# Performance work log

Hardware: AMD Instinct MI355X
Metric: run time of the kernel (lower is better)

## Reference

```python
import jax, jax.numpy as jnp
import numpy as np

B, N_PTS, M_ROIS = 2, 8192, 2048
C_IN, O, H, NS = 128, 256, 4, 32
RADIUS = 1.6
BN_EPS = 1e-5
SCALE = 10.0  # point cloud extent


def setup_inputs() -> dict:
    key = jax.random.key(0)
    ks = jax.random.split(key, 20)
    f32 = jnp.float32
    Cg = C_IN + 3  # grouper concats relative xyz to features

    def kaiming(k, shape, fan_in):
        return jax.random.normal(k, shape, f32) * np.sqrt(2.0 / fan_in)

    inp = {
        "xyz": jax.random.uniform(ks[0], (B, N_PTS, 3), f32) * SCALE,
        "new_xyz": jax.random.uniform(ks[1], (B, M_ROIS, 3), f32) * SCALE,
        "features": jax.random.normal(ks[2], (B, C_IN, N_PTS), f32),
        # conv1d (kernel=1, no bias) weights, torch layout (out, in)
        "pos_w": kaiming(ks[3], (O, 3), 3),
        "key_w": kaiming(ks[4], (O, Cg), Cg),
        "val_w1": kaiming(ks[5], (O, Cg), Cg),
        "bn1_g": jnp.ones((O,), f32), "bn1_b": jnp.zeros((O,), f32),
        "val_w2": kaiming(ks[6], (O, O), O),
        "bn2_g": jnp.ones((O,), f32), "bn2_b": jnp.zeros((O,), f32),
        "attn_w": kaiming(ks[7], (H, O), O),
        # sigmoid-gated coefficient linears (no bias)
        "kc_w": kaiming(ks[8], (O, O), O),
        "qc_w": kaiming(ks[9], (O, O), O),
        "qkc_w": kaiming(ks[10], (O, O), O),
        "vc_w": kaiming(ks[11], (O, O), O),
        # cls/reg weight MLPs: Linear(O,O//2)+ReLU, Linear(O//2,1)+Sigmoid
        "cls_w1": kaiming(ks[12], (O // 2, O), O), "cls_b1": jnp.zeros((O // 2,), f32),
        "cls_w2": kaiming(ks[13], (1, O // 2), O // 2), "cls_b2": jnp.zeros((1,), f32),
        "reg_w1": kaiming(ks[14], (O // 2, O), O), "reg_b1": jnp.zeros((O // 2,), f32),
        "reg_w2": kaiming(ks[15], (1, O // 2), O // 2), "reg_b2": jnp.zeros((1,), f32),
    }
    return inp


def _bn(x, g, b):
    # eval-mode BatchNorm1d with running_mean=0, running_var=1 (init state)
    return g[None, :, None] * (x * (1.0 / np.sqrt(1.0 + BN_EPS))) + b[None, :, None]


def _conv1x1(w, x):  # (O,C) x (M,C,NS) -> (M,O,NS)
    return jnp.einsum('oc,mcn->mon', w, x)


def _ball_group(pts, q):
    # ball query: first NS points within RADIUS of each query (pad with first hit)
    n_tot = pts.shape[0]
    d2 = jnp.sum((q[:, None, :] - pts[None, :, :]) ** 2, axis=-1)  # (M, Ntot)
    order = jnp.where(d2 < RADIUS ** 2, jnp.arange(n_tot, dtype=jnp.int32), n_tot)
    neg_vals, idx = jax.lax.top_k(-order, NS)  # smallest indices among in-ball pts
    valid = (-neg_vals) < n_tot
    idx = jnp.where(valid, idx, idx[:, :1])  # pad with first neighbor
    has_any = valid[:, :1]
    idx = jnp.where(has_any, idx, 0)  # empty balls -> point 0
    return idx, ~has_any[:, 0]


def reference(xyz, new_xyz, features, pos_w, key_w, val_w1, bn1_g, bn1_b,
              val_w2, bn2_g, bn2_b, attn_w, kc_w, qc_w, qkc_w, vc_w,
              cls_w1, cls_b1, cls_w2, cls_b2, reg_w1, reg_b1, reg_w2, reg_b2):
    pts = xyz.reshape(-1, 3)                                   # (Ntot, 3)
    feats = features.transpose(0, 2, 1).reshape(-1, C_IN)      # (Ntot, C)
    q = new_xyz.reshape(-1, 3)                                 # (M, 3)

    idx, empty_mask = _ball_group(pts, q)                      # (M, NS)
    gx = pts[idx] - q[:, None, :]                              # relative xyz (M,NS,3)
    gxt = gx.transpose(0, 2, 1)                                # (M,3,NS)
    gf = jnp.concatenate([gx, feats[idx]], axis=-1).transpose(0, 2, 1)  # (M,C+3,NS)

    pos = jax.nn.relu(_conv1x1(pos_w, gxt))                    # (M,O,NS)
    key = jax.nn.relu(_conv1x1(key_w, gf))                     # (M,O,NS)
    v = jax.nn.relu(_bn(_conv1x1(val_w1, gf), bn1_g, bn1_b))
    val = jax.nn.relu(_bn(_conv1x1(val_w2, v), bn2_g, bn2_b))  # (M,O,NS)
    pos_key = pos * key

    sig = jax.nn.sigmoid
    v_c = sig(pos.mean(2) @ vc_w.T)                            # (M,O)
    q_c = sig(pos.mean(2) @ qc_w.T)
    k_c = sig(key.mean(2) @ kc_w.T)
    qk_c = sig(pos_key.mean(2) @ qkc_w.T)

    val = val + pos * v_c[:, :, None]
    attn_emb = pos * q_c[:, :, None] + key * k_c[:, :, None] + pos_key * qk_c[:, :, None]
    attn = jax.nn.softmax(jnp.einsum('ho,mon->mhn', attn_w, attn_emb), axis=-1)  # (M,H,NS)

    m = val.shape[0]
    vh = val.reshape(m, H, O // H, NS)
    new_features = jnp.einsum('mhdn,mhn->mhd', vh, attn).reshape(m, O)  # (M,O)

    def gate(x, w1, b1, w2, b2):
        return sig(jax.nn.relu(x @ w1.T + b1) @ w2.T + b2)

    cls_features = new_features * gate(new_features, cls_w1, cls_b1, cls_w2, cls_b2)
    reg_features = new_features * gate(new_features, reg_w1, reg_b1, reg_w2, reg_b2)
    return new_features, cls_features, reg_features
```

## Files before the change

kernel.cpp:

```cpp
#include <hip/hip_runtime.h>

#define DI __device__ __forceinline__

typedef __attribute__((ext_vector_type(8))) short bf16x8;
typedef __attribute__((ext_vector_type(4))) short s16x4;
typedef __attribute__((ext_vector_type(4))) float f32x4;

DI short f2bs(float x){ unsigned u = __float_as_uint(x);
  return (short)((u + 0x7FFF + ((u >> 16) & 1)) >> 16); }
DI float bs2f(short s){ return __uint_as_float(((unsigned)(unsigned short)s) << 16); }
DI f32x4 MFMA(bf16x8 a, bf16x8 b, f32x4 c){
  return __builtin_amdgcn_mfma_f32_16x16x32_bf16(a, b, c, 0, 0, 0);
}

constexpr int NP   = 8192;
constexpr int NTOT = 16384;
constexpr int M    = 4096;
constexpr int C    = 128;
constexpr int O    = 256;
constexpr int NS   = 32;
constexpr int H    = 4;
constexpr int KP   = 160;
constexpr int GFS  = 168;
constexpr int VS   = 264;
constexpr int NSP  = 34;
constexpr float BNS = 0.99999500003749969f;

__global__ __launch_bounds__(256) void k_prep(
    const float* __restrict__ feat,
    const float* __restrict__ kw, const float* __restrict__ v1w,
    const float* __restrict__ v2w,
    const float* __restrict__ vcw, const float* __restrict__ qcw,
    const float* __restrict__ kcw, const float* __restrict__ qkcw,
    const float* __restrict__ cw1, const float* __restrict__ rw1,
    const float* __restrict__ xyz, const float* __restrict__ nxyz,
    short* __restrict__ fT,
    short* __restrict__ keyP, short* __restrict__ v1P,
    short* __restrict__ v2b,
    short* __restrict__ gw,
    short* __restrict__ cw1b, short* __restrict__ rw1b,
    float* __restrict__ xyz4, float* __restrict__ nxyz4)
{
  __shared__ float tile[128][65];
  int blk = blockIdx.x;
  int t = threadIdx.x;
  if(blk < 256){
    int b  = blk >> 7;
    int n0 = (blk & 127) << 6;
    int nn = t & 63, c4 = t >> 6;
    const float* src = feat + (size_t)b * C * NP;
    for(int i = 0; i < 32; i++){
      int c = c4 * 32 + i;
      tile[c][nn] = src[(size_t)c * NP + n0 + nn];
    }
    __syncthreads();
    int c2 = t & 127, nb = t >> 7;
    for(int j = 0; j < 32; j++){
      int n = nb + j * 2;
      fT[((size_t)(b * NP + n0 + n)) * C + c2] = f2bs(tile[c2][n]);
    }
    return;
  }
  int i = (blk - 256) * 256 + t;
  if(i < O * KP){
    int o = i / KP, k = i % KP;
    float a = 0.0f, b = 0.0f;
    if(k < 128){ a = kw[o*131 + 3 + k]; b = v1w[o*131 + 3 + k]; }
    else if(k < 131){ a = kw[o*131 + (k - 128)]; b = v1w[o*131 + (k - 128)]; }
    keyP[i] = f2bs(a);
    v1P[i]  = f2bs(b);
  }
  if(i < O * O){
    v2b[i] = f2bs(v2w[i]);
    gw[0*O*O + i] = f2bs(vcw[i]);
    gw[1*O*O + i] = f2bs(qcw[i]);
    gw[2*O*O + i] = f2bs(kcw[i]);
    gw[3*O*O + i] = f2bs(qkcw[i]);
  }
  if(i < (O/2) * O){
    cw1b[i] = f2bs(cw1[i]);
    rw1b[i] = f2bs(rw1[i]);
  }
  if(i < NTOT){
    xyz4[i*4+0] = xyz[i*3+0];
    xyz4[i*4+1] = xyz[i*3+1];
    xyz4[i*4+2] = xyz[i*3+2];
    xyz4[i*4+3] = 0.0f;
  }
  if(i < M){
    nxyz4[i*4+0] = nxyz[i*3+0];
    nxyz4[i*4+1] = nxyz[i*3+1];
    nxyz4[i*4+2] = nxyz[i*3+2];
    nxyz4[i*4+3] = 0.0f;
  }
}

__global__ __launch_bounds__(256) void k_ballq(const float* __restrict__ xyz4,
                                               const float* __restrict__ nxyz4,
                                               int* __restrict__ idxo,
                                               float* __restrict__ gxo){
#pragma clang fp contract(off)
  int m = blockIdx.x;
  int t = threadIdx.x;
  int w = t >> 6, lane = t & 63;
  float qx = nxyz4[m*4+0], qy = nxyz4[m*4+1], qz = nxyz4[m*4+2];
  __shared__ int sel[NS];
  __shared__ int wcnt[2][4];
  int cnt = 0;
  int par = 0;
  for(int base = 0; base < NTOT; base += 256){
    int p = base + t;
    const float4 pt = *(const float4*)(xyz4 + (size_t)p*4);
    float dx = qx - pt.x, dy = qy - pt.y, dz = qz - pt.z;
    float d2 = dx*dx + dy*dy;
    d2 = d2 + dz*dz;
    bool pred = d2 < 2.56f;
    unsigned long long bal = __ballot(pred);
    if(lane == 0) wcnt[par][w] = __popcll(bal);
    __syncthreads();
    int c0 = wcnt[par][0], c1 = wcnt[par][1], c2 = wcnt[par][2], c3 = wcnt[par][3];
    int off = cnt + ((w > 0) ? c0 : 0) + ((w > 1) ? c1 : 0) + ((w > 2) ? c2 : 0);
    if(pred){
      int pos = off + __popcll(bal & ((1ull << lane) - 1ull));
      if(pos < NS) sel[pos] = p;
    }
    cnt += c0 + c1 + c2 + c3;
    par ^= 1;
    if(cnt >= NS) break;
  }
  __syncthreads();
  if(t < NS){
    int s = 0;
    if(cnt > 0) s = (t < cnt) ? sel[t] : sel[0];
    idxo[m*NS + t] = s;
    const float4 ps = *(const float4*)(xyz4 + (size_t)s*4);
    gxo[(m*NS+t)*3+0] = ps.x - qx;
    gxo[(m*NS+t)*3+1] = ps.y - qy;
    gxo[(m*NS+t)*3+2] = ps.z - qz;
  }
}

__global__ __launch_bounds__(256, 5) void k_conv(
    const short* __restrict__ fT,
    const short* __restrict__ keyP, const short* __restrict__ v1P,
    const short* __restrict__ v2b,
    const float* __restrict__ posw,
    const float* __restrict__ g1, const float* __restrict__ b1,
    const float* __restrict__ g2, const float* __restrict__ b2,
    const int* __restrict__ idxw, const float* __restrict__ gxw,
    short* __restrict__ keyT, short* __restrict__ valT,
    short* __restrict__ mPos, short* __restrict__ mKey, short* __restrict__ mPK,
    int q0)
{
  int lq = blockIdx.x, q = q0 + lq, t = threadIdx.x;
  int w = t >> 6, l = t & 63;
  int col = l & 15, kq = l >> 4;
  int ro = w * 64;
  __shared__ __align__(16) short gf[NS * GFS];
  __shared__ __align__(16) short buf[O * NSP];
  __shared__ float gxs[NS * 4];
  __shared__ int  sel[NS];
  if(t < NS){
    sel[t] = idxw[q*NS + t];
    gxs[t*4+0] = gxw[(q*NS+t)*3+0];
    gxs[t*4+1] = gxw[(q*NS+t)*3+1];
    gxs[t*4+2] = gxw[(q*NS+t)*3+2];
    gxs[t*4+3] = 0.0f;
  }
  __syncthreads();
  for(int i = 0; i < 8; i++){
    int n = w*8 + i;
    int p = sel[n];
    *(unsigned*)&gf[n*GFS + l*2] = *(const unsigned*)(fT + (size_t)p * C + l*2);
  }
  {
    int n = t & 31, kk = (t >> 5) * 4;
    for(int j = 0; j < 4; j++){
      int k = kk + j;
      float v = (k < 3) ? gxs[n*4 + k] : 0.0f;
      gf[n*GFS + 128 + k] = f2bs(v);
    }
  }
  __syncthreads();

  f32x4 acc[4][2];
  const f32x4 vzero = {0.0f, 0.0f, 0.0f, 0.0f};

  for(int mt=0;mt<4;mt++) for(int nt=0;nt<2;nt++) acc[mt][nt] = vzero;
  for(int ks = 0; ks < 5; ks++){
    bf16x8 b0 = *(const bf16x8*)&gf[col*GFS + ks*32 + kq*8];
    bf16x8 b1v = *(const bf16x8*)&gf[(16+col)*GFS + ks*32 + kq*8];
    for(int mt = 0; mt < 4; mt++){
      bf16x8 a = *(const bf16x8*)(keyP + (size_t)(ro + mt*16 + col)*KP + ks*32 + kq*8);
      acc[mt][0] = MFMA(a, b0, acc[mt][0]);
      acc[mt][1] = MFMA(a, b1v, acc[mt][1]);
    }
  }
  for(int mt=0;mt<4;mt++) for(int nt=0;nt<2;nt++)
    for(int r=0;r<4;r++){
      int o = ro + mt*16 + kq*4 + r;
      int n = nt*16 + col;
      buf[o*NSP + n] = f2bs(fmaxf(acc[mt][nt][r], 0.0f));
    }
  for(int mt=0;mt<4;mt++){
    for(int r=0;r<4;r++){
      int o = ro + mt*16 + kq*4 + r;
      float w0 = posw[o*3+0], w1 = posw[o*3+1], w2 = posw[o*3+2];
      float sp = 0, sk = 0, spk = 0;
      for(int nt=0;nt<2;nt++){
        int n = nt*16 + col;
        float p = fmaxf(w0*gxs[n*4+0] + w1*gxs[n*4+1] + w2*gxs[n*4+2], 0.0f);
        float v = fmaxf(acc[mt][nt][r], 0.0f);
        sp += p; sk += v; spk += p*v;
      }
      for(int msk=1; msk<16; msk<<=1){
        sp += __shfl_xor(sp, msk); sk += __shfl_xor(sk, msk); spk += __shfl_xor(spk, msk);
      }
      if(col == 0){
        mPos[lq*O+o] = f2bs(sp  * 0.03125f);
        mKey[lq*O+o] = f2bs(sk  * 0.03125f);
        mPK [lq*O+o] = f2bs(spk * 0.03125f);
      }
    }
  }
  __syncthreads();
  {
    uint vv[16];
    #pragma unroll
    for(int j=0;j<16;j++) vv[j] = *(const uint*)&buf[t*NSP + j*2];
    uint4* dst = (uint4*)(keyT + ((size_t)lq*O + t)*NS);
    dst[0] = make_uint4(vv[0],vv[1],vv[2],vv[3]);
    dst[1] = make_uint4(vv[4],vv[5],vv[6],vv[7]);
    dst[2] = make_uint4(vv[8],vv[9],vv[10],vv[11]);
    dst[3] = make_uint4(vv[12],vv[13],vv[14],vv[15]);
  }

  for(int mt=0;mt<4;mt++) for(int nt=0;nt<2;nt++) acc[mt][nt] = vzero;
  for(int ks = 0; ks < 5; ks++){
    bf16x8 b0 = *(const bf16x8*)&gf[col*GFS + ks*32 + kq*8];
    bf16x8 b1v = *(const bf16x8*)&gf[(16+col)*GFS + ks*32 + kq*8];
    for(int mt = 0; mt < 4; mt++){
      bf16x8 a = *(const bf16x8*)(v1P + (size_t)(ro + mt*16 + col)*KP + ks*32 + kq*8);
      acc[mt][0] = MFMA(a, b0, acc[mt][0]);
      acc[mt][1] = MFMA(a, b1v, acc[mt][1]);
    }
  }
  __syncthreads();
  for(int mt=0;mt<4;mt++){
    int o0 = ro + mt*16 + kq*4;
    float gg[4], bb[4];
    for(int r=0;r<4;r++){ gg[r] = g1[o0+r]; bb[r] = b1[o0+r]; }
    for(int nt=0;nt<2;nt++){
      s16x4 pk;
      for(int r=0;r<4;r++)
        pk[r] = f2bs(fmaxf(gg[r]*(acc[mt][nt][r] * BNS) + bb[r], 0.0f));
      int n = nt*16 + col;
      *(s16x4*)&buf[n*VS + o0] = pk;
    }
  }
  __syncthreads();

  for(int mt=0;mt<4;mt++) for(int nt=0;nt<2;nt++) acc[mt][nt] = vzero;
  for(int ks = 0; ks < 8; ks++){
    bf16x8 b0 = *(const bf16x8*)&buf[col*VS + ks*32 + kq*8];
    bf16x8 b1v = *(const bf16x8*)&buf[(16+col)*VS + ks*32 + kq*8];
    for(int mt = 0; mt < 4; mt++){
      bf16x8 a = *(const bf16x8*)(v2b + (size_t)(ro + mt*16 + col)*O + ks*32 + kq*8);
      acc[mt][0] = MFMA(a, b0, acc[mt][0]);
      acc[mt][1] = MFMA(a, b1v, acc[mt][1]);
    }
  }
  __syncthreads();
  for(int mt=0;mt<4;mt++){
    int o0 = ro + mt*16 + kq*4;
    float gg[4], bb[4];
    for(int r=0;r<4;r++){ gg[r] = g2[o0+r]; bb[r] = b2[o0+r]; }
    for(int nt=0;nt<2;nt++){
      int n = nt*16 + col;
      for(int r=0;r<4;r++)
        buf[(o0+r)*NSP + n] = f2bs(fmaxf(gg[r]*(acc[mt][nt][r] * BNS) + bb[r], 0.0f));
    }
  }
  __syncthreads();
  {
    uint vv[16];
    #pragma unroll
    for(int j=0;j<16;j++) vv[j] = *(const uint*)&buf[t*NSP + j*2];
    uint4* dst = (uint4*)(valT + ((size_t)lq*O + t)*NS);
    dst[0] = make_uint4(vv[0],vv[1],vv[2],vv[3]);
    dst[1] = make_uint4(vv[4],vv[5],vv[6],vv[7]);
    dst[2] = make_uint4(vv[8],vv[9],vv[10],vv[11]);
    dst[3] = make_uint4(vv[12],vv[13],vv[14],vv[15]);
  }
}

__global__ __launch_bounds__(256) void k_gates(
    const short* __restrict__ mPos, const short* __restrict__ mKey,
    const short* __restrict__ mPK, const short* __restrict__ gw,
    float* __restrict__ gates)
{
  int t = threadIdx.x, w = t >> 6, l = t & 63, col = l & 15, kq = l >> 4;
  int lq0 = blockIdx.x * 16;
  const short* A  = (w < 2) ? mPos : ((w == 2) ? mKey : mPK);
  const short* Wg = gw + (size_t)w * O * O;
  f32x4 acc[16];
  const f32x4 vzero = {0.0f,0.0f,0.0f,0.0f};
  for(int i=0;i<16;i++) acc[i] = vzero;
  for(int ks = 0; ks < 8; ks++){
    bf16x8 av = *(const bf16x8*)(A + (size_t)(lq0 + col)*O + ks*32 + kq*8);
    for(int nt = 0; nt < 16; nt++){
      bf16x8 bv = *(const bf16x8*)(Wg + (size_t)(nt*16 + col)*O + ks*32 + kq*8);
      acc[nt] = MFMA(av, bv, acc[nt]);
    }
  }
  for(int nt=0;nt<16;nt++) for(int r=0;r<4;r++){
    int lqq = lq0 + kq*4 + r;
    int oo = nt*16 + col;
    gates[((size_t)lqq*4 + w)*O + oo] = 1.0f / (1.0f + expf(-acc[nt][r]));
  }
}

__global__ __launch_bounds__(256) void k_attn(
    const short* __restrict__ keyT, const short* __restrict__ valT,
    const float* __restrict__ gxw, const float* __restrict__ posw,
    const float* __restrict__ attw, const float* __restrict__ gates,
    float* __restrict__ outNF, int q0)
{
  int lq = blockIdx.x, q = q0 + lq, t = threadIdx.x;
  __shared__ short embL[O * NSP];
  __shared__ float attnL[H * NS];
  __shared__ float gxs[NS * 3];
  __shared__ float partial[256];
  if(t < 96) gxs[t] = gxw[q*96 + t];
  float vc  = gates[((size_t)lq*4 + 0)*O + t];
  float qc  = gates[((size_t)lq*4 + 1)*O + t];
  float kc  = gates[((size_t)lq*4 + 2)*O + t];
  float qkc = gates[((size_t)lq*4 + 3)*O + t];
  float pw0 = posw[t*3+0], pw1 = posw[t*3+1], pw2 = posw[t*3+2];
  __syncthreads();
  float posr[NS];
  #pragma unroll
  for(int n = 0; n < NS; n++)
    posr[n] = fmaxf(pw0*gxs[n*3] + pw1*gxs[n*3+1] + pw2*gxs[n*3+2], 0.0f);
  {
    const short* kp = keyT + ((size_t)lq*O + t)*NS;
    #pragma unroll
    for(int g = 0; g < 4; g++){
      bf16x8 kg = *(const bf16x8*)(kp + g*8);
      #pragma unroll
      for(int jj = 0; jj < 4; jj++){
        int n0 = g*8 + jj*2;
        float kA = bs2f(kg[jj*2]),   kB = bs2f(kg[jj*2+1]);
        float eA = posr[n0]*qc   + kA*kc + posr[n0]*kA*qkc;
        float eB = posr[n0+1]*qc + kB*kc + posr[n0+1]*kB*qkc;
        unsigned pk = (unsigned)(unsigned short)f2bs(eA)
                    | ((unsigned)(unsigned short)f2bs(eB) << 16);
        *(unsigned*)&embL[t*NSP + n0] = pk;
      }
    }
  }
  __syncthreads();
  {
    int idx = t & 127, h = idx >> 5, n = idx & 31, half = t >> 7;
    const float* aw = attw + h*O + half*128;
    const short* eb = embL + (size_t)half*128*NSP + n;
    float s0=0, s1=0, s2=0, s3=0;
    for(int o = 0; o < 128; o += 4){
      s0 += aw[o+0] * bs2f(eb[(o+0)*NSP]);
      s1 += aw[o+1] * bs2f(eb[(o+1)*NSP]);
      s2 += aw[o+2] * bs2f(eb[(o+2)*NSP]);
      s3 += aw[o+3] * bs2f(eb[(o+3)*NSP]);
    }
    partial[t] = (s0 + s1) + (s2 + s3);
  }
  __syncthreads();
  if(t < 128){
    int h = t >> 5, n = t & 31;
    float s = partial[t] + partial[t + 128];
    float mx = s;
    for(int msk=1; msk<32; msk<<=1) mx = fmaxf(mx, __shfl_xor(mx, msk));
    float e = expf(s - mx);
    float sum = e;
    for(int msk=1; msk<32; msk<<=1) sum += __shfl_xor(sum, msk);
    attnL[h*NS + n] = e / sum;
  }
  __syncthreads();
  {
    const short* vp = valT + ((size_t)lq*O + t)*NS;
    int hh = t >> 6;
    float nf = 0;
    #pragma unroll
    for(int g = 0; g < 4; g++){
      bf16x8 vg = *(const bf16x8*)(vp + g*8);
      #pragma unroll
      for(int j = 0; j < 8; j++){
        int n = g*8 + j;
        nf += (bs2f(vg[j]) + posr[n]*vc) * attnL[hh*NS + n];
      }
    }
    outNF[(size_t)q*O + t] = nf;
  }
}

__global__ __launch_bounds__(256) void k_fgate(
    const float* __restrict__ nf,
    const short* __restrict__ cw1b, const float* __restrict__ cb1,
    const float* __restrict__ cw2, const float* __restrict__ cb2,
    const short* __restrict__ rw1b, const float* __restrict__ rb1,
    const float* __restrict__ rw2, const float* __restrict__ rb2,
    float* __restrict__ outC, float* __restrict__ outR)
{
  int t = threadIdx.x, w = t >> 6, l = t & 63, col = l & 15, kq = l >> 4;
  int q0 = blockIdx.x * 64;
  __shared__ float sC[64], sR[64];
  f32x4 acc[16];
  const f32x4 vzero = {0.0f,0.0f,0.0f,0.0f};
  for(int i=0;i<16;i++) acc[i] = vzero;
  int arow = q0 + w*16 + col;
  for(int ks = 0; ks < 8; ks++){
    union { bf16x8 v; short e[8]; } u;
    const float* ap = nf + (size_t)arow*O + ks*32 + kq*8;
    for(int j = 0; j < 8; j++) u.e[j] = f2bs(ap[j]);
    for(int nt = 0; nt < 16; nt++){
      const short* W1 = (nt < 8) ? cw1b : rw1b;
      int j = (nt & 7)*16 + col;
      bf16x8 bv = *(const bf16x8*)(W1 + (size_t)j*O + ks*32 + kq*8);
      acc[nt] = MFMA(u.v, bv, acc[nt]);
    }
  }
  for(int r = 0; r < 4; r++){
    float pc = 0, pr = 0;
    for(int nt = 0; nt < 8; nt++){
      int j = nt*16 + col;
      pc += fmaxf(acc[nt][r] + cb1[j], 0.0f) * cw2[j];
    }
    for(int nt = 8; nt < 16; nt++){
      int j = (nt - 8)*16 + col;
      pr += fmaxf(acc[nt][r] + rb1[j], 0.0f) * rw2[j];
    }
    for(int msk=1; msk<16; msk<<=1){ pc += __shfl_xor(pc, msk); pr += __shfl_xor(pr, msk); }
    if(col == 0){
      int qq = w*16 + kq*4 + r;
      sC[qq] = 1.0f / (1.0f + expf(-(pc + cb2[0])));
      sR[qq] = 1.0f / (1.0f + expf(-(pr + rb2[0])));
    }
  }
  __syncthreads();
  for(int it = 0; it < 16; it++){
    int qq = it*4 + w;
    float sc = sC[qq], sr = sR[qq];
    const f32x4 nv = *(const f32x4*)(nf + (size_t)(q0 + qq)*O + l*4);
    f32x4 oc, orr;
    #pragma unroll
    for(int r=0;r<4;r++){ oc[r] = nv[r]*sc; orr[r] = nv[r]*sr; }
    *(f32x4*)(outC + (size_t)(q0 + qq)*O + l*4) = oc;
    *(f32x4*)(outR + (size_t)(q0 + qq)*O + l*4) = orr;
  }
}

extern "C" void kernel_launch(void* const* d_in, const int* in_sizes, int n_in,
                              void* d_out, int out_size, void* d_ws, size_t ws_size,
                              hipStream_t stream)
{
  const float* xyz  = (const float*)d_in[0];
  const float* nxyz = (const float*)d_in[1];
  const float* feat = (const float*)d_in[2];
  const float* posw = (const float*)d_in[3];
  const float* keyw = (const float*)d_in[4];
  const float* v1w  = (const float*)d_in[5];
  const float* bn1g = (const float*)d_in[6];
  const float* bn1b = (const float*)d_in[7];
  const float* v2w  = (const float*)d_in[8];
  const float* bn2g = (const float*)d_in[9];
  const float* bn2b = (const float*)d_in[10];
  const float* attw = (const float*)d_in[11];
  const float* kcw  = (const float*)d_in[12];
  const float* qcw  = (const float*)d_in[13];
  const float* qkcw = (const float*)d_in[14];
  const float* vcw  = (const float*)d_in[15];
  const float* cw1  = (const float*)d_in[16];
  const float* cb1  = (const float*)d_in[17];
  const float* cw2  = (const float*)d_in[18];
  const float* cb2  = (const float*)d_in[19];
  const float* rw1  = (const float*)d_in[20];
  const float* rb1  = (const float*)d_in[21];
  const float* rw2  = (const float*)d_in[22];
  const float* rb2  = (const float*)d_in[23];

  const size_t fixedB = 12000000;
  const size_t perQ   = 40960;
  int Q = 64;
  for(int cand : {4096, 2048, 1024, 512, 256, 128}){
    if(fixedB + (size_t)cand*perQ <= ws_size){ Q = cand; break; }
  }

  char* p = (char*)d_ws;
  auto alloc = [&](size_t bytes){ char* r = p; p += (bytes + 255) & ~size_t(255); return r; };
  short* fT    = (short*)alloc((size_t)NTOT*C*2);
  short* keyP  = (short*)alloc((size_t)O*KP*2);
  short* v1P   = (short*)alloc((size_t)O*KP*2);
  short* v2b   = (short*)alloc((size_t)O*O*2);
  short* gw    = (short*)alloc((size_t)4*O*O*2);
  short* cw1b  = (short*)alloc((size_t)(O/2)*O*2);
  short* rw1b  = (short*)alloc((size_t)(O/2)*O*2);
  int*   idxw  = (int*)  alloc((size_t)M*NS*4);
  float* gxw   = (float*)alloc((size_t)M*NS*3*4);
  float* xyz4  = (float*)alloc((size_t)NTOT*4*4);
  float* nxyz4 = (float*)alloc((size_t)M*4*4);
  short* keyT  = (short*)alloc((size_t)Q*O*NS*2);
  short* valT  = (short*)alloc((size_t)Q*O*NS*2);
  short* mPos  = (short*)alloc((size_t)Q*O*2);
  short* mKey  = (short*)alloc((size_t)Q*O*2);
  short* mPK   = (short*)alloc((size_t)Q*O*2);
  float* gates = (float*)alloc((size_t)Q*4*O*4);

  float* outNF = (float*)d_out;
  float* outC  = outNF + (size_t)M*O;
  float* outR  = outC  + (size_t)M*O;

  k_prep     <<<512, 256, 0, stream>>>(feat, keyw, v1w, v2w, vcw, qcw, kcw, qkcw,
                                       cw1, rw1, xyz, nxyz,
                                       fT, keyP, v1P, v2b, gw, cw1b, rw1b, xyz4, nxyz4);
  k_ballq    <<<M,   256, 0, stream>>>(xyz4, nxyz4, idxw, gxw);
  for(int q0 = 0; q0 < M; q0 += Q){
    k_conv  <<<Q,    256, 0, stream>>>(fT, keyP, v1P, v2b,
                                       posw, bn1g, bn1b, bn2g, bn2b,
                                       idxw, gxw, keyT, valT, mPos, mKey, mPK, q0);
    k_gates <<<Q/16, 256, 0, stream>>>(mPos, mKey, mPK, gw, gates);
    k_attn  <<<Q,    256, 0, stream>>>(keyT, valT, gxw, posw, attw, gates, outNF, q0);
  }
  k_fgate   <<<M/64, 256, 0, stream>>>(outNF, cw1b, cb1, cw2, cb2, rw1b, rb1, rw2, rb2, outC, outR);
}
```

Baseline: 363.8 us.

## Fuse conv, gate, and attention kernels into one per-ROI mega kernel

Merges k_conv, k_gates and k_attn into one kernel per query. The gate linears, attention embedding, softmax and value reduction are now computed in shared memory and registers instead of round-tripping keyT/valT/means/gates through global memory, and the chunked launch loop is removed. The cost is that gate matvecs now run as scalar FMAs per block rather than batched MFMA. Extra shared scratch and register use may also reduce occupancy.

Result: slower. 749.1 us (+105.9%).

```diff
diff --git a/kernel.cpp b/kernel.cpp
--- a/kernel.cpp
+++ b/kernel.cpp
@@ -140,19 +140,18 @@
   }
 }
 
-__global__ __launch_bounds__(256, 5) void k_conv(
+__global__ __launch_bounds__(256, 5) void k_mega(
     const short* __restrict__ fT,
     const short* __restrict__ keyP, const short* __restrict__ v1P,
-    const short* __restrict__ v2b,
+    const short* __restrict__ v2b, const short* __restrict__ gw,
     const float* __restrict__ posw,
     const float* __restrict__ g1, const float* __restrict__ b1,
     const float* __restrict__ g2, const float* __restrict__ b2,
+    const float* __restrict__ attw,
     const int* __restrict__ idxw, const float* __restrict__ gxw,
-    short* __restrict__ keyT, short* __restrict__ valT,
-    short* __restrict__ mPos, short* __restrict__ mKey, short* __restrict__ mPK,
-    int q0)
+    float* __restrict__ outNF)
 {
-  int lq = blockIdx.x, q = q0 + lq, t = threadIdx.x;
+  int q = blockIdx.x, t = threadIdx.x;
   int w = t >> 6, l = t & 63;
   int col = l & 15, kq = l >> 4;
   int ro = w * 64;
@@ -160,6 +159,14 @@
   __shared__ __align__(16) short buf[O * NSP];
   __shared__ float gxs[NS * 4];
   __shared__ int  sel[NS];
+  __shared__ __align__(16) char scr1[1536];
+  __shared__ __align__(16) float scr2[384];
+  short* meanL  = (short*)scr1;
+  float* partial= (float*)scr1;
+  float* nfL    = (float*)scr1;
+  float* vcL    = scr2;
+  float* attnL  = scr2 + 256;
+
   if(t < NS){
     sel[t] = idxw[q*NS + t];
     gxs[t*4+0] = gxw[(q*NS+t)*3+0];
@@ -217,23 +224,88 @@
         sp += __shfl_xor(sp, msk); sk += __shfl_xor(sk, msk); spk += __shfl_xor(spk, msk);
       }
       if(col == 0){
-        mPos[lq*O+o] = f2bs(sp  * 0.03125f);
-        mKey[lq*O+o] = f2bs(sk  * 0.03125f);
-        mPK [lq*O+o] = f2bs(spk * 0.03125f);
+        meanL[0*O+o] = f2bs(sp  * 0.03125f);
+        meanL[1*O+o] = f2bs(sk  * 0.03125f);
+        meanL[2*O+o] = f2bs(spk * 0.03125f);
       }
     }
   }
   __syncthreads();
+
+  float qcv, kcv, qkcv;
   {
-    uint vv[16];
+    const short* g0 = gw + 0*O*O + t*O;
+    const short* g1r = gw + 1*O*O + t*O;
+    const short* g2r = gw + 2*O*O + t*O;
+    const short* g3r = gw + 3*O*O + t*O;
+    float av=0, aq=0, ak=0, aqk=0;
+    for(int c8 = 0; c8 < 32; c8++){
+      bf16x8 mp = *(const bf16x8*)&meanL[0*O + c8*8];
+      bf16x8 mk = *(const bf16x8*)&meanL[1*O + c8*8];
+      bf16x8 mq = *(const bf16x8*)&meanL[2*O + c8*8];
+      bf16x8 w0 = *(const bf16x8*)(g0  + c8*8);
+      bf16x8 w1 = *(const bf16x8*)(g1r + c8*8);
+      bf16x8 w2 = *(const bf16x8*)(g2r + c8*8);
+      bf16x8 w3 = *(const bf16x8*)(g3r + c8*8);
+      #pragma unroll
+      for(int j = 0; j < 8; j++){
+        float p = bs2f(mp[j]), k = bs2f(mk[j]), pk = bs2f(mq[j]);
+        av  += bs2f(w0[j]) * p;
+        aq  += bs2f(w1[j]) * p;
+        ak  += bs2f(w2[j]) * k;
+        aqk += bs2f(w3[j]) * pk;
+      }
+    }
+    vcL[t] = 1.0f / (1.0f + expf(-av));
+    qcv  = 1.0f / (1.0f + expf(-aq));
+    kcv  = 1.0f / (1.0f + expf(-ak));
+    qkcv = 1.0f / (1.0f + expf(-aqk));
+  }
+
+  {
+    float w0 = posw[t*3+0], w1 = posw[t*3+1], w2 = posw[t*3+2];
     #pragma unroll
-    for(int j=0;j<16;j++) vv[j] = *(const uint*)&buf[t*NSP + j*2];
-    uint4* dst = (uint4*)(keyT + ((size_t)lq*O + t)*NS);
-    dst[0] = make_uint4(vv[0],vv[1],vv[2],vv[3]);
-    dst[1] = make_uint4(vv[4],vv[5],vv[6],vv[7]);
-    dst[2] = make_uint4(vv[8],vv[9],vv[10],vv[11]);
-    dst[3] = make_uint4(vv[12],vv[13],vv[14],vv[15]);
-  }
+    for(int j = 0; j < 16; j++){
+      unsigned kk2 = *(const unsigned*)&buf[t*NSP + j*2];
+      int n0 = j*2;
+      float kA = bs2f((short)(kk2 & 0xFFFF));
+      float kB = bs2f((short)(kk2 >> 16));
+      float pA = fmaxf(w0*gxs[n0*4+0]     + w1*gxs[n0*4+1]     + w2*gxs[n0*4+2], 0.0f);
+      float pB = fmaxf(w0*gxs[(n0+1)*4+0] + w1*gxs[(n0+1)*4+1] + w2*gxs[(n0+1)*4+2], 0.0f);
+      float eA = pA*qcv + kA*kcv + pA*kA*qkcv;
+      float eB = pB*qcv + kB*kcv + pB*kB*qkcv;
+      unsigned pk = (unsigned)(unsigned short)f2bs(eA)
+                  | ((unsigned)(unsigned short)f2bs(eB) << 16);
+      *(unsigned*)&buf[t*NSP + j*2] = pk;
+    }
+  }
+  __syncthreads();
+
+  {
+    int idx = t & 127, h = idx >> 5, n = idx & 31, half = t >> 7;
+    const float* aw = attw + h*O + half*128;
+    const short* eb = buf + (size_t)half*128*NSP + n;
+    float s0=0, s1=0, s2=0, s3=0;
+    for(int o = 0; o < 128; o += 4){
+      s0 += aw[o+0] * bs2f(eb[(o+0)*NSP]);
+      s1 += aw[o+1] * bs2f(eb[(o+1)*NSP]);
+      s2 += aw[o+2] * bs2f(eb[(o+2)*NSP]);
+      s3 += aw[o+3] * bs2f(eb[(o+3)*NSP]);
+    }
+    partial[t] = (s0 + s1) + (s2 + s3);
+  }
+  __syncthreads();
+  if(t < 128){
+    int h = t >> 5, n = t & 31;
+    float s = partial[t] + partial[t + 128];
+    float mx = s;
+    for(int msk=1; msk<32; msk<<=1) mx = fmaxf(mx, __shfl_xor(mx, msk));
+    float e = expf(s - mx);
+    float sum = e;
+    for(int msk=1; msk<32; msk<<=1) sum += __shfl_xor(sum, msk);
+    attnL[h*NS + n] = e / sum;
+  }
+  __syncthreads();
 
   for(int mt=0;mt<4;mt++) for(int nt=0;nt<2;nt++) acc[mt][nt] = vzero;
   for(int ks = 0; ks < 5; ks++){
@@ -245,7 +317,6 @@
       acc[mt][1] = MFMA(a, b1v, acc[mt][1]);
     }
   }
-  __syncthreads();
   for(int mt=0;mt<4;mt++){
     int o0 = ro + mt*16 + kq*4;
     float gg[4], bb[4];
@@ -270,136 +341,30 @@
       acc[mt][1] = MFMA(a, b1v, acc[mt][1]);
     }
   }
-  __syncthreads();
-  for(int mt=0;mt<4;mt++){
-    int o0 = ro + mt*16 + kq*4;
-    float gg[4], bb[4];
-    for(int r=0;r<4;r++){ gg[r] = g2[o0+r]; bb[r] = b2[o0+r]; }
-    for(int nt=0;nt<2;nt++){
-      int n = nt*16 + col;
-      for(int r=0;r<4;r++)
-        buf[(o0+r)*NSP + n] = f2bs(fmaxf(gg[r]*(acc[mt][nt][r] * BNS) + bb[r], 0.0f));
-    }
-  }
-  __syncthreads();
   {
-    uint vv[16];
-    #pragma unroll
-    for(int j=0;j<16;j++) vv[j] = *(const uint*)&buf[t*NSP + j*2];
-    uint4* dst = (uint4*)(valT + ((size_t)lq*O + t)*NS);
-    dst[0] = make_uint4(vv[0],vv[1],vv[2],vv[3]);
-    dst[1] = make_uint4(vv[4],vv[5],vv[6],vv[7]);
-    dst[2] = make_uint4(vv[8],vv[9],vv[10],vv[11]);
-    dst[3] = make_uint4(vv[12],vv[13],vv[14],vv[15]);
-  }
-}
-
-__global__ __launch_bounds__(256) void k_gates(
-    const short* __restrict__ mPos, const short* __restrict__ mKey,
-    const short* __restrict__ mPK, const short* __restrict__ gw,
-    float* __restrict__ gates)
-{
-  int t = threadIdx.x, w = t >> 6, l = t & 63, col = l & 15, kq = l >> 4;
-  int lq0 = blockIdx.x * 16;
-  const short* A  = (w < 2) ? mPos : ((w == 2) ? mKey : mPK);
-  const short* Wg = gw + (size_t)w * O * O;
-  f32x4 acc[16];
-  const f32x4 vzero = {0.0f,0.0f,0.0f,0.0f};
-  for(int i=0;i<16;i++) acc[i] = vzero;
-  for(int ks = 0; ks < 8; ks++){
-    bf16x8 av = *(const bf16x8*)(A + (size_t)(lq0 + col)*O + ks*32 + kq*8);
-    for(int nt = 0; nt < 16; nt++){
-      bf16x8 bv = *(const bf16x8*)(Wg + (size_t)(nt*16 + col)*O + ks*32 + kq*8);
-      acc[nt] = MFMA(av, bv, acc[nt]);
-    }
-  }
-  for(int nt=0;nt<16;nt++) for(int r=0;r<4;r++){
-    int lqq = lq0 + kq*4 + r;
-    int oo = nt*16 + col;
-    gates[((size_t)lqq*4 + w)*O + oo] = 1.0f / (1.0f + expf(-acc[nt][r]));
-  }
-}
-
-__global__ __launch_bounds__(256) void k_attn(
-    const short* __restrict__ keyT, const short* __restrict__ valT,
-    const float* __restrict__ gxw, const float* __restrict__ posw,
-    const float* __restrict__ attw, const float* __restrict__ gates,
-    float* __restrict__ outNF, int q0)
-{
-  int lq = blockIdx.x, q = q0 + lq, t = threadIdx.x;
-  __shared__ short embL[O * NSP];
-  __shared__ float attnL[H * NS];
-  __shared__ float gxs[NS * 3];
-  __shared__ float partial[256];
-  if(t < 96) gxs[t] = gxw[q*96 + t];
-  float vc  = gates[((size_t)lq*4 + 0)*O + t];
-  float qc  = gates[((size_t)lq*4 + 1)*O + t];
-  float kc  = gates[((size_t)lq*4 + 2)*O + t];
-  float qkc = gates[((size_t)lq*4 + 3)*O + t];
-  float pw0 = posw[t*3+0], pw1 = posw[t*3+1], pw2 = posw[t*3+2];
-  __syncthreads();
-  float posr[NS];
-  #pragma unroll
-  for(int n = 0; n < NS; n++)
-    posr[n] = fmaxf(pw0*gxs[n*3] + pw1*gxs[n*3+1] + pw2*gxs[n*3+2], 0.0f);
-  {
-    const short* kp = keyT + ((size_t)lq*O + t)*NS;
-    #pragma unroll
-    for(int g = 0; g < 4; g++){
-      bf16x8 kg = *(const bf16x8*)(kp + g*8);
-      #pragma unroll
-      for(int jj = 0; jj < 4; jj++){
-        int n0 = g*8 + jj*2;
-        float kA = bs2f(kg[jj*2]),   kB = bs2f(kg[jj*2+1]);
-        float eA = posr[n0]*qc   + kA*kc + posr[n0]*kA*qkc;
-        float eB = posr[n0+1]*qc + kB*kc + posr[n0+1]*kB*qkc;
-        unsigned pk = (unsigned)(unsigned short)f2bs(eA)
-                    | ((unsigned)(unsigned short)f2bs(eB) << 16);
-        *(unsigned*)&embL[t*NSP + n0] = pk;
+    float a0 = attnL[w*NS + col];
+    float a1 = attnL[w*NS + 16 + col];
+    for(int mt=0;mt<4;mt++){
+      int o0 = ro + mt*16 + kq*4;
+      float gg[4], bb[4];
+      for(int r=0;r<4;r++){ gg[r] = g2[o0+r]; bb[r] = b2[o0+r]; }
+      for(int r=0;r<4;r++){
+        int o = o0 + r;
+        float w0 = posw[o*3+0], w1 = posw[o*3+1], w2 = posw[o*3+2];
+        float vc = vcL[o];
+        int n0 = col, n1 = 16 + col;
+        float p0 = fmaxf(w0*gxs[n0*4+0] + w1*gxs[n0*4+1] + w2*gxs[n0*4+2], 0.0f);
+        float p1 = fmaxf(w0*gxs[n1*4+0] + w1*gxs[n1*4+1] + w2*gxs[n1*4+2], 0.0f);
+        float val0 = fmaxf(gg[r]*(acc[mt][0][r] * BNS) + bb[r], 0.0f);
+        float val1 = fmaxf(gg[r]*(acc[mt][1][r] * BNS) + bb[r], 0.0f);
+        float nf = (val0 + p0*vc) * a0 + (val1 + p1*vc) * a1;
+        for(int msk=1; msk<16; msk<<=1) nf += __shfl_xor(nf, msk);
+        if(col == 0) nfL[o] = nf;
       }
     }
   }
   __syncthreads();
-  {
-    int idx = t & 127, h = idx >> 5, n = idx & 31, half = t >> 7;
-    const float* aw = attw + h*O + half*128;
-    const short* eb = embL + (size_t)half*128*NSP + n;
-    float s0=0, s1=0, s2=0, s3=0;
-    for(int o = 0; o < 128; o += 4){
-      s0 += aw[o+0] * bs2f(eb[(o+0)*NSP]);
-      s1 += aw[o+1] * bs2f(eb[(o+1)*NSP]);
-      s2 += aw[o+2] * bs2f(eb[(o+2)*NSP]);
-      s3 += aw[o+3] * bs2f(eb[(o+3)*NSP]);
-    }
-    partial[t] = (s0 + s1) + (s2 + s3);
-  }
-  __syncthreads();
-  if(t < 128){
-    int h = t >> 5, n = t & 31;
-    float s = partial[t] + partial[t + 128];
-    float mx = s;
-    for(int msk=1; msk<32; msk<<=1) mx = fmaxf(mx, __shfl_xor(mx, msk));
-    float e = expf(s - mx);
-    float sum = e;
-    for(int msk=1; msk<32; msk<<=1) sum += __shfl_xor(sum, msk);
-    attnL[h*NS + n] = e / sum;
-  }
-  __syncthreads();
-  {
-    const short* vp = valT + ((size_t)lq*O + t)*NS;
-    int hh = t >> 6;
-    float nf = 0;
-    #pragma unroll
-    for(int g = 0; g < 4; g++){
-      bf16x8 vg = *(const bf16x8*)(vp + g*8);
-      #pragma unroll
-      for(int j = 0; j < 8; j++){
-        int n = g*8 + j;
-        nf += (bs2f(vg[j]) + posr[n]*vc) * attnL[hh*NS + n];
-      }
-    }
-    outNF[(size_t)q*O + t] = nf;
-  }
+  outNF[(size_t)q*O + t] = nfL[t];
 }
 
 __global__ __launch_bounds__(256) void k_fgate(
@@ -487,13 +452,6 @@
   const float* rw2  = (const float*)d_in[22];
   const float* rb2  = (const float*)d_in[23];
 
-  const size_t fixedB = 12000000;
-  const size_t perQ   = 40960;
-  int Q = 64;
-  for(int cand : {4096, 2048, 1024, 512, 256, 128}){
-    if(fixedB + (size_t)cand*perQ <= ws_size){ Q = cand; break; }
-  }
-
   char* p = (char*)d_ws;
   auto alloc = [&](size_t bytes){ char* r = p; p += (bytes + 255) & ~size_t(255); return r; };
   short* fT    = (short*)alloc((size_t)NTOT*C*2);
@@ -507,27 +465,17 @@
   float* gxw   = (float*)alloc((size_t)M*NS*3*4);
   float* xyz4  = (float*)alloc((size_t)NTOT*4*4);
   float* nxyz4 = (float*)alloc((size_t)M*4*4);
-  short* keyT  = (short*)alloc((size_t)Q*O*NS*2);
-  short* valT  = (short*)alloc((size_t)Q*O*NS*2);
-  short* mPos  = (short*)alloc((size_t)Q*O*2);
-  short* mKey  = (short*)alloc((size_t)Q*O*2);
-  short* mPK   = (short*)alloc((size_t)Q*O*2);
-  float* gates = (float*)alloc((size_t)Q*4*O*4);
 
   float* outNF = (float*)d_out;
   float* outC  = outNF + (size_t)M*O;
   float* outR  = outC  + (size_t)M*O;
 
-  k_prep     <<<512, 256, 0, stream>>>(feat, keyw, v1w, v2w, vcw, qcw, kcw, qkcw,
-                                       cw1, rw1, xyz, nxyz,
-                                       fT, keyP, v1P, v2b, gw, cw1b, rw1b, xyz4, nxyz4);
-  k_ballq    <<<M,   256, 0, stream>>>(xyz4, nxyz4, idxw, gxw);
-  for(int q0 = 0; q0 < M; q0 += Q){
-    k_conv  <<<Q,    256, 0, stream>>>(fT, keyP, v1P, v2b,
-                                       posw, bn1g, bn1b, bn2g, bn2b,
-                                       idxw, gxw, keyT, valT, mPos, mKey, mPK, q0);
-    k_gates <<<Q/16, 256, 0, stream>>>(mPos, mKey, mPK, gw, gates);
-    k_attn  <<<Q,    256, 0, stream>>>(keyT, valT, gxw, posw, attw, gates, outNF, q0);
-  }
-  k_fgate   <<<M/64, 256, 0, stream>>>(outNF, cw1b, cb1, cw2, cb2, rw1b, rb1, rw2, rb2, outC, outR);
-}
+  k_prep  <<<512, 256, 0, stream>>>(feat, keyw, v1w, v2w, vcw, qcw, kcw, qkcw,
+                                    cw1, rw1, xyz, nxyz,
+                                    fT, keyP, v1P, v2b, gw, cw1b, rw1b, xyz4, nxyz4);
+  k_ballq <<<M,   256, 0, stream>>>(xyz4, nxyz4, idxw, gxw);
+  k_mega  <<<M,   256, 0, stream>>>(fT, keyP, v1P, v2b, gw,
+                                    posw, bn1g, bn1b, bn2g, bn2b, attw,
+                                    idxw, gxw, outNF);
+  k_fgate <<<M/64, 256, 0, stream>>>(outNF, cw1b, cb1, cw2, cb2, rw1b, rb1, rw2, rb2, outC, outR);
+}
```
